# Optimization experiments

Hardware: AMD Instinct MI355X
Metric: run time of the kernel (lower is better)

The kernel has to match this reference:

```python
import jax, jax.numpy as jnp
import numpy as np

UNITS = 512
MODELS = 64
BATCH = 64
INPUT_DIM = 512


def setup_inputs() -> dict:
    key = jax.random.key(0)
    ks = jax.random.split(key, 6)
    scale = 0.05  # keep gates in a sane range like 'random_normal' init
    return {
        "inputs": jax.random.normal(ks[0], (MODELS, BATCH, INPUT_DIM), jnp.float32),
        "h_tm1": jax.random.normal(ks[1], (MODELS, BATCH, UNITS), jnp.float32),
        "c_tm1": jax.random.normal(ks[2], (MODELS, BATCH, UNITS), jnp.float32),
        "kernel": jax.random.normal(ks[3], (MODELS, INPUT_DIM, 4 * UNITS), jnp.float32) * scale,
        "recurrent_kernel": jax.random.normal(ks[4], (MODELS, UNITS, 4 * UNITS), jnp.float32) * scale,
        "bias": jax.random.normal(ks[5], (MODELS, 1, 4 * UNITS), jnp.float32) * scale,
    }


def reference(inputs, h_tm1, c_tm1, kernel, recurrent_kernel, bias):
    # batched over the models axis: [m,b,d] @ [m,d,4u] -> [m,b,4u]
    z = jnp.einsum('mbd,mdu->mbu', inputs, kernel)
    z = z + jnp.einsum('mbh,mhu->mbu', h_tm1, recurrent_kernel)
    z = z + bias  # broadcasts over batch
    z0, z1, z2, z3 = jnp.split(z, 4, axis=-1)
    i = jax.nn.sigmoid(z0)
    f = jax.nn.sigmoid(z1)
    c = f * c_tm1 + i * jnp.tanh(z2)
    o = jax.nn.sigmoid(z3)
    h = o * jnp.tanh(c)
    return (h, h, c)
```

## Files before the change

kernel.cpp:

```cpp
#include <hip/hip_runtime.h>
#include <hip/hip_bf16.h>

#define MODELS 64
#define BATCH 64
#define IN_DIM 512
#define UNITS 512
#define NCOLS 2048
#define GRAN_PER_TENSOR (MODELS * 16 * 4 * 64)

typedef __attribute__((ext_vector_type(8))) short short8;
typedef __attribute__((ext_vector_type(4))) float f32x4;

static __device__ __forceinline__ short f2bf(float f) {
    return __builtin_bit_cast(short, __float2bfloat16(f));
}
static __device__ __forceinline__ float sigmoidf_(float x) {
    return 1.0f / (1.0f + __expf(-x));
}
static __device__ __forceinline__ float tanhf_(float x) {
    float e = __expf(-2.0f * fabsf(x));
    float r = (1.0f - e) / (1.0f + e);
    return copysignf(r, x);
}

__global__ __launch_bounds__(256) void prepack_A_kernel(
    const float* __restrict__ x, const float* __restrict__ h,
    short8* __restrict__ P)
{
    const int t = blockIdx.x * 256 + threadIdx.x;
    const int tensor = t >> 18;
    const int r = t & (GRAN_PER_TENSOR - 1);
    const int kg = r & 3;
    const int row = (r >> 2) & 63;
    const int ks = (r >> 8) & 15;
    const int m = r >> 12;
    const float* src = (tensor ? h : x) + ((size_t)(m * 64 + row) * 512 + ks * 32 + kg * 8);
    f32x4 a0 = *(const f32x4*)src;
    f32x4 a1 = *(const f32x4*)(src + 4);
    short8 v;
    v[0] = f2bf(a0[0]); v[1] = f2bf(a0[1]); v[2] = f2bf(a0[2]); v[3] = f2bf(a0[3]);
    v[4] = f2bf(a1[0]); v[5] = f2bf(a1[1]); v[6] = f2bf(a1[2]); v[7] = f2bf(a1[3]);
    P[(size_t)tensor * GRAN_PER_TENSOR + (size_t)((m * 16 + ks) * 4 + kg) * 64 + row] = v;
}

__global__ __launch_bounds__(512, 4) void lstm_main_kernel(
    const float* __restrict__ c_tm1,
    const float* __restrict__ kernel_,
    const float* __restrict__ rkernel,
    const float* __restrict__ bias,
    const short8* __restrict__ Pa,
    float* __restrict__ out)
{
    __shared__ float lds[16384];

    const int bid = blockIdx.x;
    const int m = bid >> 3;
    const int u0 = (bid & 7) * 64;
    const int tid = threadIdx.x;
    const int wave = tid >> 6;
    const int lane = tid & 63;
    const int col16 = lane & 15;
    const int kq = lane >> 4;

    const float* wbase[2] = { kernel_ + (size_t)m * IN_DIM * NCOLS,
                              rkernel + (size_t)m * UNITS * NCOLS };
    const short8* pabase[2] = { Pa + (size_t)m * 4096,
                                Pa + GRAN_PER_TENSOR + (size_t)m * 4096 };

    f32x4 acc[4][2];
#pragma unroll
    for (int bt = 0; bt < 4; ++bt)
#pragma unroll
        for (int c = 0; c < 2; ++c) acc[bt][c] = (f32x4){0.f, 0.f, 0.f, 0.f};

    auto STAGE = [&](int step, int bufsel) {
        const float* wb = wbase[step >> 4];
        const int krow0 = (step & 15) * 32;
#pragma unroll
        for (int j = 0; j < 4; ++j) {
            const int k = j * 8 + wave;
            const float* src = wb + (size_t)(krow0 + k) * NCOLS
                             + kq * 512 + u0 + ((col16 ^ (j << 1)) * 4);
            float* dst = lds + bufsel * 8192 + k * 256;
            __builtin_amdgcn_global_load_lds(
                (const __attribute__((address_space(1))) void*)src,
                (__attribute__((address_space(3))) void*)dst, 16, 0, 0);
        }
    };
    auto LOADA = [&](int step, short8* af) {
        const short8* pb = pabase[step >> 4] + (size_t)((step & 15) * 4 + kq) * 64 + col16;
#pragma unroll
        for (int bt = 0; bt < 4; ++bt)
            asm volatile("global_load_dwordx4 %0, %1, off"
                         : "=v"(af[bt]) : "v"(pb + bt * 16) : "memory");
    };
    auto COMPUTE = [&](int bufsel, short8* af) {
        const float* lb = lds + bufsel * 8192;
#pragma unroll
        for (int c = 0; c < 2; ++c) {
            const int cb = (wave * 2 + c) * 16 + col16;
            const int cbs = cb ^ (kq << 3);
            short8 bfr;
#pragma unroll
            for (int i = 0; i < 8; ++i)
                bfr[i] = f2bf(lb[(kq * 8 + i) * 256 + cbs]);
#pragma unroll
            for (int bt = 0; bt < 4; ++bt)
                acc[bt][c] = __builtin_amdgcn_mfma_f32_16x16x32_bf16(
                    af[bt], bfr, acc[bt][c], 0, 0, 0);
        }
    };

    short8 afA[4], afB[4];
    STAGE(0, 0);
    LOADA(0, afA);

    for (int tp = 0; tp < 16; ++tp) {
        const int te = 2 * tp;
        STAGE(te + 1, 1);
        LOADA(te + 1, afB);
        asm volatile("s_waitcnt vmcnt(8)"
                     : "+v"(afA[0]), "+v"(afA[1]), "+v"(afA[2]), "+v"(afA[3]) :: "memory");
        asm volatile("s_barrier" ::: "memory");
        COMPUTE(0, afA);
        asm volatile("s_waitcnt lgkmcnt(0)" ::: "memory");
        asm volatile("s_barrier" ::: "memory");
        if (tp < 15) {
            STAGE(te + 2, 0);
            LOADA(te + 2, afA);
            asm volatile("s_waitcnt vmcnt(8)"
                         : "+v"(afB[0]), "+v"(afB[1]), "+v"(afB[2]), "+v"(afB[3]) :: "memory");
        } else {
            asm volatile("s_waitcnt vmcnt(0)"
                         : "+v"(afB[0]), "+v"(afB[1]), "+v"(afB[2]), "+v"(afB[3]) :: "memory");
        }
        asm volatile("s_barrier" ::: "memory");
        COMPUTE(1, afB);
        asm volatile("s_waitcnt lgkmcnt(0)" ::: "memory");
        asm volatile("s_barrier" ::: "memory");
    }

#pragma unroll
    for (int bt = 0; bt < 4; ++bt)
#pragma unroll
        for (int c = 0; c < 2; ++c)
#pragma unroll
            for (int r = 0; r < 4; ++r)
                lds[(size_t)(bt * 16 + kq * 4 + r) * 256 + (wave * 2 + c) * 16 + col16] =
                    acc[bt][c][r];
    __syncthreads();

    const int b = tid >> 3;
    const int ug = (tid & 7) * 8;

    float zi[8], zf[8], zc[8], zo[8];
    *(f32x4*)&zi[0] = *(const f32x4*)&lds[b * 256 + 0 + ug];
    *(f32x4*)&zi[4] = *(const f32x4*)&lds[b * 256 + 0 + ug + 4];
    *(f32x4*)&zf[0] = *(const f32x4*)&lds[b * 256 + 64 + ug];
    *(f32x4*)&zf[4] = *(const f32x4*)&lds[b * 256 + 64 + ug + 4];
    *(f32x4*)&zc[0] = *(const f32x4*)&lds[b * 256 + 128 + ug];
    *(f32x4*)&zc[4] = *(const f32x4*)&lds[b * 256 + 128 + ug + 4];
    *(f32x4*)&zo[0] = *(const f32x4*)&lds[b * 256 + 192 + ug];
    *(f32x4*)&zo[4] = *(const f32x4*)&lds[b * 256 + 192 + ug + 4];

    const float* bb = bias + (size_t)m * NCOLS;
    float bi[8], bf_[8], bc[8], bo[8];
    *(f32x4*)&bi[0] = *(const f32x4*)&bb[0 * 512 + u0 + ug];
    *(f32x4*)&bi[4] = *(const f32x4*)&bb[0 * 512 + u0 + ug + 4];
    *(f32x4*)&bf_[0] = *(const f32x4*)&bb[1 * 512 + u0 + ug];
    *(f32x4*)&bf_[4] = *(const f32x4*)&bb[1 * 512 + u0 + ug + 4];
    *(f32x4*)&bc[0] = *(const f32x4*)&bb[2 * 512 + u0 + ug];
    *(f32x4*)&bc[4] = *(const f32x4*)&bb[2 * 512 + u0 + ug + 4];
    *(f32x4*)&bo[0] = *(const f32x4*)&bb[3 * 512 + u0 + ug];
    *(f32x4*)&bo[4] = *(const f32x4*)&bb[3 * 512 + u0 + ug + 4];

    const size_t cidx = (size_t)m * (BATCH * UNITS) + (size_t)b * UNITS + u0 + ug;
    float cp[8];
    *(f32x4*)&cp[0] = *(const f32x4*)&c_tm1[cidx];
    *(f32x4*)&cp[4] = *(const f32x4*)&c_tm1[cidx + 4];

    float hv[8], cv[8];
#pragma unroll
    for (int j = 0; j < 8; ++j) {
        const float ig = sigmoidf_(zi[j] + bi[j]);
        const float fg = sigmoidf_(zf[j] + bf_[j]);
        const float cand = tanhf_(zc[j] + bc[j]);
        const float og = sigmoidf_(zo[j] + bo[j]);
        const float c = fg * cp[j] + ig * cand;
        cv[j] = c;
        hv[j] = og * tanhf_(c);
    }

    float* hout0 = out;
    float* hout1 = out + (size_t)MODELS * BATCH * UNITS;
    float* cout = out + 2 * (size_t)MODELS * BATCH * UNITS;
    *(f32x4*)&hout0[cidx] = *(const f32x4*)&hv[0];
    *(f32x4*)&hout0[cidx + 4] = *(const f32x4*)&hv[4];
    *(f32x4*)&hout1[cidx] = *(const f32x4*)&hv[0];
    *(f32x4*)&hout1[cidx + 4] = *(const f32x4*)&hv[4];
    *(f32x4*)&cout[cidx] = *(const f32x4*)&cv[0];
    *(f32x4*)&cout[cidx + 4] = *(const f32x4*)&cv[4];
}

extern "C" void kernel_launch(void* const* d_in, const int* in_sizes, int n_in,
                              void* d_out, int out_size, void* d_ws, size_t ws_size,
                              hipStream_t stream) {
    const float* inputs = (const float*)d_in[0];
    const float* h_tm1 = (const float*)d_in[1];
    const float* c_tm1 = (const float*)d_in[2];
    const float* kernel_ = (const float*)d_in[3];
    const float* rkernel = (const float*)d_in[4];
    const float* bias = (const float*)d_in[5];
    float* out = (float*)d_out;

    short8* P = (short8*)d_ws;
    hipLaunchKernelGGL(prepack_A_kernel, dim3(2 * GRAN_PER_TENSOR / 256), dim3(256),
                       0, stream, inputs, h_tm1, P);
    hipLaunchKernelGGL(lstm_main_kernel, dim3(MODELS * 8), dim3(512), 0, stream,
                       c_tm1, kernel_, rkernel, bias, P, out);
}
```

Measured before the change: 136.6 us.

## Give each wave a private LDS weight slice and drop block barriers

Each wave now stages its own gate-column slice of the weight tile into a private LDS region. This lets the main K loop drop its block-wide s_barrier and lgkmcnt waits and rely only on per-wave vmcnt ordering plus scheduling fences. Block indices are remapped so that consecutive blocks cover different models, which spreads concurrent weight streams across memory. The z tile written out for the epilogue gets a padded row stride to cut LDS bank conflicts. The risk is that LDS reuse within a wave now depends on implicit ordering between ds_read and the async global_load_lds writes.

```diff
diff --git a/kernel.cpp b/kernel.cpp
--- a/kernel.cpp
+++ b/kernel.cpp
@@ -7,6 +7,7 @@
 #define UNITS 512
 #define NCOLS 2048
 #define GRAN_PER_TENSOR (MODELS * 16 * 4 * 64)
+#define ZSTRIDE 260
 
 typedef __attribute__((ext_vector_type(8))) short short8;
 typedef __attribute__((ext_vector_type(4))) float f32x4;
@@ -43,7 +44,7 @@
     P[(size_t)tensor * GRAN_PER_TENSOR + (size_t)((m * 16 + ks) * 4 + kg) * 64 + row] = v;
 }
 
-__global__ __launch_bounds__(512, 4) void lstm_main_kernel(
+__global__ __launch_bounds__(512, 4) void lstm_wave_kernel(
     const float* __restrict__ c_tm1,
     const float* __restrict__ kernel_,
     const float* __restrict__ rkernel,
@@ -51,63 +52,68 @@
     const short8* __restrict__ Pa,
     float* __restrict__ out)
 {
-    __shared__ float lds[16384];
+    __shared__ float lds[16640];
 
     const int bid = blockIdx.x;
-    const int m = bid >> 3;
-    const int u0 = (bid & 7) * 64;
+    const int slot = bid >> 3;
+    const int m = ((slot >> 3) << 3) | (bid & 7);
+    const int u0 = (slot & 7) * 64;
+
     const int tid = threadIdx.x;
     const int wave = tid >> 6;
     const int lane = tid & 63;
     const int col16 = lane & 15;
     const int kq = lane >> 4;
+    const int g = wave >> 1;
+    const int uh = wave & 1;
+    const int colf = g * 512 + u0 + uh * 32;
+    const int l3 = lane >> 3, l7 = lane & 7;
 
     const float* wbase[2] = { kernel_ + (size_t)m * IN_DIM * NCOLS,
                               rkernel + (size_t)m * UNITS * NCOLS };
     const short8* pabase[2] = { Pa + (size_t)m * 4096,
                                 Pa + GRAN_PER_TENSOR + (size_t)m * 4096 };
 
+    float* wlds = lds + wave * 2048;
+
     f32x4 acc[4][2];
 #pragma unroll
     for (int bt = 0; bt < 4; ++bt)
 #pragma unroll
-        for (int c = 0; c < 2; ++c) acc[bt][c] = (f32x4){0.f, 0.f, 0.f, 0.f};
+        for (int ct = 0; ct < 2; ++ct) acc[bt][ct] = (f32x4){0.f, 0.f, 0.f, 0.f};
 
     auto STAGE = [&](int step, int bufsel) {
-        const float* wb = wbase[step >> 4];
-        const int krow0 = (step & 15) * 32;
+        const char* wbc = (const char*)(wbase[step >> 4]
+                          + (size_t)(step & 15) * 32 * NCOLS + colf);
 #pragma unroll
         for (int j = 0; j < 4; ++j) {
-            const int k = j * 8 + wave;
-            const float* src = wb + (size_t)(krow0 + k) * NCOLS
-                             + kq * 512 + u0 + ((col16 ^ (j << 1)) * 4);
-            float* dst = lds + bufsel * 8192 + k * 256;
+            const char* src = wbc + l3 * 8192 + (((l7 << 4) ^ (j << 5))) + j * 65536;
+            float* dst = wlds + bufsel * 1024 + j * 256;
             __builtin_amdgcn_global_load_lds(
                 (const __attribute__((address_space(1))) void*)src,
                 (__attribute__((address_space(3))) void*)dst, 16, 0, 0);
         }
     };
-    auto LOADA = [&](int step, short8* af) {
+    auto LOADA = [&](int step, short8 (&af)[4]) {
         const short8* pb = pabase[step >> 4] + (size_t)((step & 15) * 4 + kq) * 64 + col16;
 #pragma unroll
         for (int bt = 0; bt < 4; ++bt)
             asm volatile("global_load_dwordx4 %0, %1, off"
                          : "=v"(af[bt]) : "v"(pb + bt * 16) : "memory");
     };
-    auto COMPUTE = [&](int bufsel, short8* af) {
-        const float* lb = lds + bufsel * 8192;
-#pragma unroll
-        for (int c = 0; c < 2; ++c) {
-            const int cb = (wave * 2 + c) * 16 + col16;
-            const int cbs = cb ^ (kq << 3);
+    auto COMPUTE = [&](int bufsel, short8 (&af)[4]) {
+        const float* lb = wlds + bufsel * 1024;
+#pragma unroll
+        for (int ct = 0; ct < 2; ++ct) {
+            const int gsw = (ct * 4 + (col16 >> 2)) ^ (kq << 1);
+            const int base = kq * 256 + gsw * 4 + (col16 & 3);
             short8 bfr;
 #pragma unroll
-            for (int i = 0; i < 8; ++i)
-                bfr[i] = f2bf(lb[(kq * 8 + i) * 256 + cbs]);
+            for (int i = 0; i < 8; ++i) bfr[i] = f2bf(lb[base + i * 32]);
 #pragma unroll
             for (int bt = 0; bt < 4; ++bt)
-                acc[bt][c] = __builtin_amdgcn_mfma_f32_16x16x32_bf16(
-                    af[bt], bfr, acc[bt][c], 0, 0, 0);
+                acc[bt][ct] = __builtin_amdgcn_mfma_f32_16x16x32_bf16(
+                    af[bt], bfr, acc[bt][ct], 0, 0, 0);
         }
     };
 
@@ -115,17 +121,16 @@
     STAGE(0, 0);
     LOADA(0, afA);
 
-    for (int tp = 0; tp < 16; ++tp) {
-        const int te = 2 * tp;
+    for (int sp = 0; sp < 16; ++sp) {
+        const int te = 2 * sp;
         STAGE(te + 1, 1);
         LOADA(te + 1, afB);
         asm volatile("s_waitcnt vmcnt(8)"
                      : "+v"(afA[0]), "+v"(afA[1]), "+v"(afA[2]), "+v"(afA[3]) :: "memory");
-        asm volatile("s_barrier" ::: "memory");
+        __builtin_amdgcn_sched_barrier(0);
         COMPUTE(0, afA);
-        asm volatile("s_waitcnt lgkmcnt(0)" ::: "memory");
-        asm volatile("s_barrier" ::: "memory");
-        if (tp < 15) {
+        __builtin_amdgcn_sched_barrier(0);
+        if (sp < 15) {
             STAGE(te + 2, 0);
             LOADA(te + 2, afA);
             asm volatile("s_waitcnt vmcnt(8)"
@@ -134,34 +139,35 @@
             asm volatile("s_waitcnt vmcnt(0)"
                          : "+v"(afB[0]), "+v"(afB[1]), "+v"(afB[2]), "+v"(afB[3]) :: "memory");
         }
-        asm volatile("s_barrier" ::: "memory");
+        __builtin_amdgcn_sched_barrier(0);
         COMPUTE(1, afB);
-        asm volatile("s_waitcnt lgkmcnt(0)" ::: "memory");
-        asm volatile("s_barrier" ::: "memory");
+        __builtin_amdgcn_sched_barrier(0);
     }
 
+    __syncthreads();
 #pragma unroll
     for (int bt = 0; bt < 4; ++bt)
 #pragma unroll
-        for (int c = 0; c < 2; ++c)
+        for (int ct = 0; ct < 2; ++ct)
 #pragma unroll
             for (int r = 0; r < 4; ++r)
-                lds[(size_t)(bt * 16 + kq * 4 + r) * 256 + (wave * 2 + c) * 16 + col16] =
-                    acc[bt][c][r];
+                lds[(size_t)(bt * 16 + kq * 4 + r) * ZSTRIDE
+                    + g * 64 + uh * 32 + ct * 16 + col16] = acc[bt][ct][r];
     __syncthreads();
 
     const int b = tid >> 3;
     const int ug = (tid & 7) * 8;
+    const float* zrow = lds + (size_t)b * ZSTRIDE;
 
     float zi[8], zf[8], zc[8], zo[8];
-    *(f32x4*)&zi[0] = *(const f32x4*)&lds[b * 256 + 0 + ug];
-    *(f32x4*)&zi[4] = *(const f32x4*)&lds[b * 256 + 0 + ug + 4];
-    *(f32x4*)&zf[0] = *(const f32x4*)&lds[b * 256 + 64 + ug];
-    *(f32x4*)&zf[4] = *(const f32x4*)&lds[b * 256 + 64 + ug + 4];
-    *(f32x4*)&zc[0] = *(const f32x4*)&lds[b * 256 + 128 + ug];
-    *(f32x4*)&zc[4] = *(const f32x4*)&lds[b * 256 + 128 + ug + 4];
-    *(f32x4*)&zo[0] = *(const f32x4*)&lds[b * 256 + 192 + ug];
-    *(f32x4*)&zo[4] = *(const f32x4*)&lds[b * 256 + 192 + ug + 4];
+    *(f32x4*)&zi[0] = *(const f32x4*)&zrow[0 + ug];
+    *(f32x4*)&zi[4] = *(const f32x4*)&zrow[0 + ug + 4];
+    *(f32x4*)&zf[0] = *(const f32x4*)&zrow[64 + ug];
+    *(f32x4*)&zf[4] = *(const f32x4*)&zrow[64 + ug + 4];
+    *(f32x4*)&zc[0] = *(const f32x4*)&zrow[128 + ug];
+    *(f32x4*)&zc[4] = *(const f32x4*)&zrow[128 + ug + 4];
+    *(f32x4*)&zo[0] = *(const f32x4*)&zrow[192 + ug];
+    *(f32x4*)&zo[4] = *(const f32x4*)&zrow[192 + ug + 4];
 
     const float* bb = bias + (size_t)m * NCOLS;
     float bi[8], bf_[8], bc[8], bo[8];
@@ -216,6 +222,6 @@
     short8* P = (short8*)d_ws;
     hipLaunchKernelGGL(prepack_A_kernel, dim3(2 * GRAN_PER_TENSOR / 256), dim3(256),
                        0, stream, inputs, h_tm1, P);
-    hipLaunchKernelGGL(lstm_main_kernel, dim3(MODELS * 8), dim3(512), 0, stream,
+    hipLaunchKernelGGL(lstm_wave_kernel, dim3(512), dim3(512), 0, stream,
                        c_tm1, kernel_, rkernel, bias, P, out);
 }
```

After: 151.7 us. +11.0%, slower.
